# Performance work log

Hardware: AMD Instinct MI355X
Metric: run time of the kernel (lower is better)

Reference implementation:

```python
import jax, jax.numpy as jnp
import numpy as np

B, L, D = 2, 2048, 1024
E = 15        # routed experts
H = D * 1     # hidden_expansion = 1
K = 3         # active experts per token
T = 1.0       # router temperature


def setup_inputs() -> dict:
    key = jax.random.key(0)
    ks = jax.random.split(key, 12)
    s = 0.02
    return {
        "x": jax.random.normal(ks[0], (B, L, D), dtype=jnp.float32),
        "router_W": jax.random.normal(ks[1], (D, E), dtype=jnp.float32) * s,
        "router_b": jnp.zeros((E,), dtype=jnp.float32),
        "sW1": jax.random.normal(ks[2], (D, H), dtype=jnp.float32) * s,
        "sb1": jnp.zeros((H,), dtype=jnp.float32),
        "sW2": jax.random.normal(ks[3], (H, D), dtype=jnp.float32) * s,
        "sb2": jnp.zeros((D,), dtype=jnp.float32),
        "eW1": jax.random.normal(ks[4], (E, D, H), dtype=jnp.float32) * s,
        "eb1": jnp.zeros((E, H), dtype=jnp.float32),
        "eW2": jax.random.normal(ks[5], (E, H, D), dtype=jnp.float32) * s,
        "eb2": jnp.zeros((E, D), dtype=jnp.float32),
    }


def reference(x, router_W, router_b, sW1, sb1, sW2, sb2, eW1, eb1, eW2, eb2):
    b, l, d = x.shape
    n = b * l
    xt = x.reshape(n, d)                                   # [N, D] tokens

    # shared expert FFN (single shared expert)
    shared = jax.nn.relu(xt @ sW1 + sb1) @ sW2 + sb2       # [N, D]

    # router: softmax over experts with temperature, top-k selection
    logits = xt @ router_W + router_b                      # [N, E]
    probs = jax.nn.softmax(logits / T, axis=-1)
    top_p, top_i = jax.lax.top_k(probs, K)                 # [N, K]

    # combine weights: zero outside top-k
    cw = jnp.zeros((n, E), dtype=probs.dtype)
    cw = cw.at[jnp.arange(n)[:, None], top_i].set(top_p)   # [N, E]

    # routed experts (dense dispatch form of gather-FFN-scatter)
    h = jax.nn.relu(jnp.einsum('nd,edh->neh', xt, eW1) + eb1)   # [N, E, H]
    ye = jnp.einsum('neh,ehd->ned', h, eW2) + eb2               # [N, E, D]
    routed = jnp.einsum('ned,ne->nd', ye, cw)                   # [N, D]

    return (shared + routed).reshape(b, l, d)
```

## Files before the change

### kernel.cpp

```cpp
#include <hip/hip_runtime.h>
#include <hip/hip_bf16.h>

#define NTOK 4096
#define DDIM 1024
#define NEXP 15
#define KTOP 3
#define NSLOT_R (NTOK*KTOP)
#define LIST_STRIDE 4096
#define BK 32
#define NT (DDIM/BK)

typedef __attribute__((ext_vector_type(4))) float f32x4;
typedef __attribute__((ext_vector_type(8))) __bf16 bf16x8;
typedef __attribute__((ext_vector_type(4))) __bf16 bf16x4;

__device__ __forceinline__ void gload_lds16(const void* g, void* l) {
    __builtin_amdgcn_global_load_lds(
        (const __attribute__((address_space(1))) void*)g,
        (__attribute__((address_space(3))) void*)l, 16, 0, 0);
}

__global__ __launch_bounds__(256) void router_kernel(
    const float* __restrict__ x, const float* __restrict__ rW,
    const float* __restrict__ rb, int* __restrict__ cnt,
    int* __restrict__ list, float* __restrict__ wslot)
{
    const int lane = threadIdx.x & 63;
    const int wid  = threadIdx.x >> 6;
    const int n    = blockIdx.x * 4 + wid;

    float xv[16];
#pragma unroll
    for (int i = 0; i < 16; ++i) xv[i] = x[(size_t)n * DDIM + lane + 64 * i];

    float p[NEXP];
#pragma unroll
    for (int e = 0; e < NEXP; ++e) {
        float s = 0.f;
#pragma unroll
        for (int i = 0; i < 16; ++i)
            s += xv[i] * rW[(size_t)(lane + 64 * i) * NEXP + e];
#pragma unroll
        for (int off = 32; off > 0; off >>= 1) s += __shfl_xor(s, off);
        p[e] = s + rb[e];
    }
    float m = p[0];
#pragma unroll
    for (int e = 1; e < NEXP; ++e) m = fmaxf(m, p[e]);
    float Z = 0.f;
#pragma unroll
    for (int e = 0; e < NEXP; ++e) { p[e] = expf(p[e] - m); Z += p[e]; }
    const float inv = 1.f / Z;

    if (lane == 0) {
        int sel0 = -1, sel1 = -1;
        for (int k = 0; k < KTOP; ++k) {
            float best = -1.f; int bi = 0;
            for (int e = 0; e < NEXP; ++e) {
                if (e == sel0 || e == sel1) continue;
                if (p[e] > best) { best = p[e]; bi = e; }
            }
            wslot[n * KTOP + k] = best * inv;
            int pos = atomicAdd(&cnt[bi], 1);
            list[bi * LIST_STRIDE + pos] = n * KTOP + k;
            if (k == 0) sel0 = bi; else sel1 = bi;
        }
    }
}

__global__ __launch_bounds__(256) void transpose_convert(
    const float* __restrict__ eW, const float* __restrict__ sW,
    __bf16* __restrict__ dst)
{
    const int bi = blockIdx.x, bj = blockIdx.y, z = blockIdx.z;
    const float* src = (z < 15) ? eW + (size_t)z * 1024 * 1024 : sW;
    __bf16* d = dst + (size_t)z * 1024 * 1024;

    __shared__ __bf16 tile[64][66];
    const int t = threadIdx.x, c = t & 63;
#pragma unroll
    for (int i = 0; i < 16; ++i) {
        int r = i * 4 + (t >> 6);
        tile[c][r] = (__bf16)src[(size_t)(bi * 64 + r) * 1024 + bj * 64 + c];
    }
    __syncthreads();
#pragma unroll
    for (int i = 0; i < 4; ++i) {
        int rr = i * 16 + (t >> 4);
        int c4 = (t & 15) * 4;
        bf16x4 v;
#pragma unroll
        for (int q = 0; q < 4; ++q) v[q] = tile[rr][c4 + q];
        *(bf16x4*)&d[(size_t)(bj * 64 + rr) * 1024 + bi * 64 + c4] = v;
    }
}

__global__ __launch_bounds__(256) void convert_x(
    const float* __restrict__ x, __bf16* __restrict__ xb)
{
    int i = (blockIdx.x * 256 + threadIdx.x) * 4;
    f32x4 v = *(const f32x4*)&x[i];
    bf16x4 o;
#pragma unroll
    for (int q = 0; q < 4; ++q) o[q] = (__bf16)v[q];
    *(bf16x4*)&xb[i] = o;
}

template<int PASS, bool ATOMIC>
__global__ __launch_bounds__(256) void ffn_pass(
    const __bf16* __restrict__ Wt,
    const float* __restrict__ eb, const float* __restrict__ sb,
    const __bf16* __restrict__ Xsrc,
    const int* __restrict__ cnt, const int* __restrict__ list,
    const float* __restrict__ wslot,
    __bf16* __restrict__ Yout,
    float* __restrict__ out)
{
    const int st = blockIdx.x;
    const int ct = blockIdx.y;
    const int e  = blockIdx.z;
    const bool shared_e = (e == NEXP);
    const int count = shared_e ? NTOK : cnt[e];
    const int s0 = st * 128;
    if (s0 >= count) return;

    const __bf16* Wp = Wt + (size_t)e * 1024 * 1024;
    const float*  bp = shared_e ? sb : eb + (size_t)e * DDIM;

    __shared__ __bf16 Wl[3][128 * BK];
    __shared__ __bf16 Xl[3][128 * BK];

    const int tid = threadIdx.x, lane = tid & 63, w = tid >> 6;
    const int wm = w >> 1, wn = w & 1, r15 = lane & 15, g = lane >> 4;

    int srcrow[2];
#pragma unroll
    for (int i = 0; i < 2; ++i) {
        int r = min(s0 + (tid >> 2) + 64 * i, count - 1);
        if (shared_e) srcrow[i] = (PASS == 1) ? r : (NSLOT_R + r);
        else { int slot = list[e * LIST_STRIDE + r]; srcrow[i] = (PASS == 1) ? (slot / KTOP) : slot; }
    }
    const int wc   = ct * 128 + (tid >> 2);
    const int gsub = (tid & 3) * 8;

    auto stage = [&](int buf, int k0) {
#pragma unroll
        for (int i = 0; i < 2; ++i) {
            gload_lds16(&Wp[(size_t)(wc + 64 * i) * 1024 + k0 + gsub],
                        &Wl[buf][(i * 64 + w * 16) * BK]);
            gload_lds16(&Xsrc[(size_t)srcrow[i] * 1024 + k0 + gsub],
                        &Xl[buf][(i * 64 + w * 16) * BK]);
        }
    };

    f32x4 acc[4][4];
#pragma unroll
    for (int a = 0; a < 4; ++a)
#pragma unroll
        for (int b = 0; b < 4; ++b) acc[a][b] = (f32x4){0.f, 0.f, 0.f, 0.f};

    stage(0, 0);
    stage(1, BK);

    for (int t = 0; t < NT; ++t) {
        if (t + 1 < NT) asm volatile("s_waitcnt vmcnt(4)" ::: "memory");
        else            asm volatile("s_waitcnt vmcnt(0)" ::: "memory");
        __builtin_amdgcn_s_barrier();
        __builtin_amdgcn_sched_barrier(0);

        const int b0 = t % 3;
        const __bf16* Wb = &Wl[b0][0];
        const __bf16* Xb = &Xl[b0][0];
        bf16x8 wf[4], xf[4];
#pragma unroll
        for (int f = 0; f < 4; ++f) {
            wf[f] = *(const bf16x8*)&Wb[(wm * 64 + f * 16 + r15) * BK + g * 8];
            xf[f] = *(const bf16x8*)&Xb[(wn * 64 + f * 16 + r15) * BK + g * 8];
        }
        if (t + 2 < NT) stage((t + 2) % 3, (t + 2) * BK);
#pragma unroll
        for (int fm = 0; fm < 4; ++fm)
#pragma unroll
            for (int fn = 0; fn < 4; ++fn)
                acc[fm][fn] = __builtin_amdgcn_mfma_f32_16x16x32_bf16(
                    wf[fm], xf[fn], acc[fm][fn], 0, 0, 0);
    }

    int  slotg[4]; bool val[4];
#pragma unroll
    for (int fn = 0; fn < 4; ++fn) {
        int sl = s0 + wn * 64 + fn * 16 + r15;
        val[fn] = (sl < count);
        int sc = min(sl, count - 1);
        slotg[fn] = shared_e ? (NSLOT_R + sc) : list[e * LIST_STRIDE + sc];
    }

    if constexpr (!ATOMIC) {
#pragma unroll
        for (int fm = 0; fm < 4; ++fm) {
            int c0 = ct * 128 + wm * 64 + fm * 16 + g * 4;
            f32x4 bias = *(const f32x4*)&bp[c0];
#pragma unroll
            for (int fn = 0; fn < 4; ++fn) if (val[fn]) {
                bf16x4 v;
#pragma unroll
                for (int q = 0; q < 4; ++q) {
                    float y = acc[fm][fn][q] + bias[q];
                    if (PASS == 1) y = fmaxf(y, 0.f);
                    v[q] = (__bf16)y;
                }
                *(bf16x4*)&Yout[(size_t)slotg[fn] * DDIM + c0] = v;
            }
        }
    } else {
        int ntok[4]; float wgt[4];
#pragma unroll
        for (int fn = 0; fn < 4; ++fn) {
            int slot = slotg[fn];
            ntok[fn] = (slot < NSLOT_R) ? (slot / KTOP) : (slot - NSLOT_R);
            wgt[fn]  = (slot < NSLOT_R) ? wslot[slot] : 1.f;
        }
#pragma unroll
        for (int fm = 0; fm < 4; ++fm) {
            int c0 = ct * 128 + wm * 64 + fm * 16 + g * 4;
            f32x4 bias = *(const f32x4*)&bp[c0];
#pragma unroll
            for (int fn = 0; fn < 4; ++fn) if (val[fn]) {
#pragma unroll
                for (int q = 0; q < 4; ++q)
                    atomicAdd(&out[(size_t)ntok[fn] * DDIM + c0 + q],
                              wgt[fn] * (acc[fm][fn][q] + bias[q]));
            }
        }
    }
}

__global__ __launch_bounds__(256) void combine_kernel(
    const __bf16* __restrict__ ybuf, const float* __restrict__ wslot,
    float* __restrict__ out)
{
    const int idx = blockIdx.x * 256 + threadIdx.x;
    const int n   = idx >> 7;
    const int d0  = (idx & 127) * 8;
    const float w0 = wslot[n * 3 + 0];
    const float w1 = wslot[n * 3 + 1];
    const float w2 = wslot[n * 3 + 2];
    bf16x8 y0 = *(const bf16x8*)&ybuf[(size_t)(n * 3 + 0) * DDIM + d0];
    bf16x8 y1 = *(const bf16x8*)&ybuf[(size_t)(n * 3 + 1) * DDIM + d0];
    bf16x8 y2 = *(const bf16x8*)&ybuf[(size_t)(n * 3 + 2) * DDIM + d0];
    bf16x8 ys = *(const bf16x8*)&ybuf[(size_t)(NSLOT_R + n) * DDIM + d0];
    float r[8];
#pragma unroll
    for (int j = 0; j < 8; ++j)
        r[j] = w0 * (float)y0[j] + w1 * (float)y1[j] + w2 * (float)y2[j] + (float)ys[j];
    f32x4 lo = {r[0], r[1], r[2], r[3]}, hi = {r[4], r[5], r[6], r[7]};
    *(f32x4*)&out[(size_t)n * DDIM + d0]     = lo;
    *(f32x4*)&out[(size_t)n * DDIM + d0 + 4] = hi;
}

extern "C" void kernel_launch(void* const* d_in, const int* in_sizes, int n_in,
                              void* d_out, int out_size, void* d_ws, size_t ws_size,
                              hipStream_t stream) {
    const float* x   = (const float*)d_in[0];
    const float* rW  = (const float*)d_in[1];
    const float* rb  = (const float*)d_in[2];
    const float* sW1 = (const float*)d_in[3];
    const float* sb1 = (const float*)d_in[4];
    const float* sW2 = (const float*)d_in[5];
    const float* sb2 = (const float*)d_in[6];
    const float* eW1 = (const float*)d_in[7];
    const float* eb1 = (const float*)d_in[8];
    const float* eW2 = (const float*)d_in[9];
    const float* eb2 = (const float*)d_in[10];
    float* out = (float*)d_out;

    const size_t MB = 1 << 20;
    char* wsb = (char*)d_ws;
    int*    cnt   = (int*)wsb;
    int*    list  = (int*)(wsb + 256);
    float*  wslot = (float*)(wsb + (512 << 10));
    __bf16* xb    = (__bf16*)(wsb + 1 * MB);

    const dim3 ggrid(NTOK / 128, DDIM / 128, NEXP + 1);

    if (ws_size >= 105 * MB) {
        __bf16* W1t  = (__bf16*)(wsb + 9 * MB);
        __bf16* W2t  = (__bf16*)(wsb + 41 * MB);
        __bf16* hbuf = (__bf16*)(wsb + 73 * MB);
        __bf16* ybuf = (__bf16*)(wsb + 9 * MB);

        hipMemsetAsync(cnt, 0, 64, stream);
        router_kernel<<<NTOK / 4, 256, 0, stream>>>(x, rW, rb, cnt, list, wslot);
        convert_x<<<NTOK * DDIM / 1024, 256, 0, stream>>>(x, xb);
        transpose_convert<<<dim3(16, 16, 16), 256, 0, stream>>>(eW1, sW1, W1t);
        transpose_convert<<<dim3(16, 16, 16), 256, 0, stream>>>(eW2, sW2, W2t);

        ffn_pass<1, false><<<ggrid, 256, 0, stream>>>(
            W1t, eb1, sb1, xb, cnt, list, nullptr, hbuf, nullptr);
        ffn_pass<2, false><<<ggrid, 256, 0, stream>>>(
            W2t, eb2, sb2, hbuf, cnt, list, nullptr, ybuf, nullptr);
        combine_kernel<<<NTOK * 128 / 256, 256, 0, stream>>>(ybuf, wslot, out);
    } else if (ws_size >= 73 * MB) {
        __bf16* Wt   = (__bf16*)(wsb + 9 * MB);
        __bf16* hbuf = (__bf16*)(wsb + 41 * MB);

        hipMemsetAsync(cnt, 0, 64, stream);
        hipMemsetAsync(d_out, 0, (size_t)out_size * sizeof(float), stream);
        router_kernel<<<NTOK / 4, 256, 0, stream>>>(x, rW, rb, cnt, list, wslot);
        convert_x<<<NTOK * DDIM / 1024, 256, 0, stream>>>(x, xb);

        transpose_convert<<<dim3(16, 16, 16), 256, 0, stream>>>(eW1, sW1, Wt);
        ffn_pass<1, false><<<ggrid, 256, 0, stream>>>(
            Wt, eb1, sb1, xb, cnt, list, nullptr, hbuf, nullptr);
        transpose_convert<<<dim3(16, 16, 16), 256, 0, stream>>>(eW2, sW2, Wt);
        ffn_pass<2, true><<<ggrid, 256, 0, stream>>>(
            Wt, eb2, sb2, hbuf, cnt, list, wslot, nullptr, out);
    }
}
```

Before: 710.9 us.

## Enlarge FFN GEMM tile to 256 tokens, fuse x conversion into router

The grouped FFN GEMM tile grows from 128x128 to 256 token rows by 128 output columns. Each wave now computes 128x64 with 32 accumulators, and the MFMA block is raised to high priority with s_setprio. Weight tiles are reused across more tokens, cutting weight traffic and the number of blocks. The bf16 conversion of x moves into the router kernel, which already loads x, removing one launch and one read of x. The costs are more registers and LDS per block, lower occupancy, and more padding waste for experts whose token counts do not fill a 256-row tile.

```diff
diff --git a/kernel.cpp b/kernel.cpp
--- a/kernel.cpp
+++ b/kernel.cpp
@@ -9,6 +9,8 @@
 #define LIST_STRIDE 4096
 #define BK 32
 #define NT (DDIM/BK)
+#define BM 256
+#define BN 128
 
 typedef __attribute__((ext_vector_type(4))) float f32x4;
 typedef __attribute__((ext_vector_type(8))) __bf16 bf16x8;
@@ -23,7 +25,8 @@
 __global__ __launch_bounds__(256) void router_kernel(
     const float* __restrict__ x, const float* __restrict__ rW,
     const float* __restrict__ rb, int* __restrict__ cnt,
-    int* __restrict__ list, float* __restrict__ wslot)
+    int* __restrict__ list, float* __restrict__ wslot,
+    __bf16* __restrict__ xb)
 {
     const int lane = threadIdx.x & 63;
     const int wid  = threadIdx.x >> 6;
@@ -32,6 +35,10 @@
     float xv[16];
 #pragma unroll
     for (int i = 0; i < 16; ++i) xv[i] = x[(size_t)n * DDIM + lane + 64 * i];
+
+#pragma unroll
+    for (int i = 0; i < 16; ++i)
+        xb[(size_t)n * DDIM + lane + 64 * i] = (__bf16)xv[i];
 
     float p[NEXP];
 #pragma unroll
@@ -93,17 +100,6 @@
         for (int q = 0; q < 4; ++q) v[q] = tile[rr][c4 + q];
         *(bf16x4*)&d[(size_t)(bj * 64 + rr) * 1024 + bi * 64 + c4] = v;
     }
-}
-
-__global__ __launch_bounds__(256) void convert_x(
-    const float* __restrict__ x, __bf16* __restrict__ xb)
-{
-    int i = (blockIdx.x * 256 + threadIdx.x) * 4;
-    f32x4 v = *(const f32x4*)&x[i];
-    bf16x4 o;
-#pragma unroll
-    for (int q = 0; q < 4; ++q) o[q] = (__bf16)v[q];
-    *(bf16x4*)&xb[i] = o;
 }
 
 template<int PASS, bool ATOMIC>
@@ -121,41 +117,42 @@
     const int e  = blockIdx.z;
     const bool shared_e = (e == NEXP);
     const int count = shared_e ? NTOK : cnt[e];
-    const int s0 = st * 128;
+    const int s0 = st * BM;
     if (s0 >= count) return;
 
     const __bf16* Wp = Wt + (size_t)e * 1024 * 1024;
     const float*  bp = shared_e ? sb : eb + (size_t)e * DDIM;
 
-    __shared__ __bf16 Wl[3][128 * BK];
-    __shared__ __bf16 Xl[3][128 * BK];
+    __shared__ __bf16 Wl[3][BN * BK];
+    __shared__ __bf16 Xl[3][BM * BK];
 
     const int tid = threadIdx.x, lane = tid & 63, w = tid >> 6;
     const int wm = w >> 1, wn = w & 1, r15 = lane & 15, g = lane >> 4;
 
-    int srcrow[2];
-#pragma unroll
-    for (int i = 0; i < 2; ++i) {
+    int srcrow[4];
+#pragma unroll
+    for (int i = 0; i < 4; ++i) {
         int r = min(s0 + (tid >> 2) + 64 * i, count - 1);
         if (shared_e) srcrow[i] = (PASS == 1) ? r : (NSLOT_R + r);
         else { int slot = list[e * LIST_STRIDE + r]; srcrow[i] = (PASS == 1) ? (slot / KTOP) : slot; }
     }
-    const int wc   = ct * 128 + (tid >> 2);
+    const int wc   = ct * BN + (tid >> 2);
     const int gsub = (tid & 3) * 8;
 
     auto stage = [&](int buf, int k0) {
 #pragma unroll
-        for (int i = 0; i < 2; ++i) {
+        for (int i = 0; i < 2; ++i)
             gload_lds16(&Wp[(size_t)(wc + 64 * i) * 1024 + k0 + gsub],
                         &Wl[buf][(i * 64 + w * 16) * BK]);
+#pragma unroll
+        for (int i = 0; i < 4; ++i)
             gload_lds16(&Xsrc[(size_t)srcrow[i] * 1024 + k0 + gsub],
                         &Xl[buf][(i * 64 + w * 16) * BK]);
-        }
     };
 
-    f32x4 acc[4][4];
-#pragma unroll
-    for (int a = 0; a < 4; ++a)
+    f32x4 acc[8][4];
+#pragma unroll
+    for (int a = 0; a < 8; ++a)
 #pragma unroll
         for (int b = 0; b < 4; ++b) acc[a][b] = (f32x4){0.f, 0.f, 0.f, 0.f};
 
@@ -163,7 +160,7 @@
     stage(1, BK);
 
     for (int t = 0; t < NT; ++t) {
-        if (t + 1 < NT) asm volatile("s_waitcnt vmcnt(4)" ::: "memory");
+        if (t + 1 < NT) asm volatile("s_waitcnt vmcnt(6)" ::: "memory");
         else            asm volatile("s_waitcnt vmcnt(0)" ::: "memory");
         __builtin_amdgcn_s_barrier();
         __builtin_amdgcn_sched_barrier(0);
@@ -171,65 +168,68 @@
         const int b0 = t % 3;
         const __bf16* Wb = &Wl[b0][0];
         const __bf16* Xb = &Xl[b0][0];
-        bf16x8 wf[4], xf[4];
-#pragma unroll
-        for (int f = 0; f < 4; ++f) {
-            wf[f] = *(const bf16x8*)&Wb[(wm * 64 + f * 16 + r15) * BK + g * 8];
-            xf[f] = *(const bf16x8*)&Xb[(wn * 64 + f * 16 + r15) * BK + g * 8];
-        }
+        bf16x8 wf[4], xf[8];
+#pragma unroll
+        for (int f = 0; f < 4; ++f)
+            wf[f] = *(const bf16x8*)&Wb[(wn * 64 + f * 16 + r15) * BK + g * 8];
+#pragma unroll
+        for (int f = 0; f < 8; ++f)
+            xf[f] = *(const bf16x8*)&Xb[(wm * 128 + f * 16 + r15) * BK + g * 8];
         if (t + 2 < NT) stage((t + 2) % 3, (t + 2) * BK);
-#pragma unroll
-        for (int fm = 0; fm < 4; ++fm)
-#pragma unroll
-            for (int fn = 0; fn < 4; ++fn)
-                acc[fm][fn] = __builtin_amdgcn_mfma_f32_16x16x32_bf16(
-                    wf[fm], xf[fn], acc[fm][fn], 0, 0, 0);
-    }
-
-    int  slotg[4]; bool val[4];
-#pragma unroll
-    for (int fn = 0; fn < 4; ++fn) {
-        int sl = s0 + wn * 64 + fn * 16 + r15;
-        val[fn] = (sl < count);
+        __builtin_amdgcn_s_setprio(1);
+#pragma unroll
+        for (int s = 0; s < 8; ++s)
+#pragma unroll
+            for (int c = 0; c < 4; ++c)
+                acc[s][c] = __builtin_amdgcn_mfma_f32_16x16x32_bf16(
+                    wf[c], xf[s], acc[s][c], 0, 0, 0);
+        __builtin_amdgcn_s_setprio(0);
+    }
+
+    int  slotg[8]; bool val[8];
+#pragma unroll
+    for (int s = 0; s < 8; ++s) {
+        int sl = s0 + wm * 128 + s * 16 + r15;
+        val[s] = (sl < count);
         int sc = min(sl, count - 1);
-        slotg[fn] = shared_e ? (NSLOT_R + sc) : list[e * LIST_STRIDE + sc];
+        slotg[s] = shared_e ? (NSLOT_R + sc) : list[e * LIST_STRIDE + sc];
     }
 
     if constexpr (!ATOMIC) {
 #pragma unroll
-        for (int fm = 0; fm < 4; ++fm) {
-            int c0 = ct * 128 + wm * 64 + fm * 16 + g * 4;
+        for (int c = 0; c < 4; ++c) {
+            int c0 = ct * BN + wn * 64 + c * 16 + g * 4;
             f32x4 bias = *(const f32x4*)&bp[c0];
 #pragma unroll
-            for (int fn = 0; fn < 4; ++fn) if (val[fn]) {
+            for (int s = 0; s < 8; ++s) if (val[s]) {
                 bf16x4 v;
 #pragma unroll
                 for (int q = 0; q < 4; ++q) {
-                    float y = acc[fm][fn][q] + bias[q];
+                    float y = acc[s][c][q] + bias[q];
                     if (PASS == 1) y = fmaxf(y, 0.f);
                     v[q] = (__bf16)y;
                 }
-                *(bf16x4*)&Yout[(size_t)slotg[fn] * DDIM + c0] = v;
+                *(bf16x4*)&Yout[(size_t)slotg[s] * DDIM + c0] = v;
             }
         }
     } else {
-        int ntok[4]; float wgt[4];
-#pragma unroll
-        for (int fn = 0; fn < 4; ++fn) {
-            int slot = slotg[fn];
-            ntok[fn] = (slot < NSLOT_R) ? (slot / KTOP) : (slot - NSLOT_R);
-            wgt[fn]  = (slot < NSLOT_R) ? wslot[slot] : 1.f;
+        int ntok[8]; float wgt[8];
+#pragma unroll
+        for (int s = 0; s < 8; ++s) {
+            int slot = slotg[s];
+            ntok[s] = (slot < NSLOT_R) ? (slot / KTOP) : (slot - NSLOT_R);
+            wgt[s]  = (slot < NSLOT_R) ? wslot[slot] : 1.f;
         }
 #pragma unroll
-        for (int fm = 0; fm < 4; ++fm) {
-            int c0 = ct * 128 + wm * 64 + fm * 16 + g * 4;
+        for (int c = 0; c < 4; ++c) {
+            int c0 = ct * BN + wn * 64 + c * 16 + g * 4;
             f32x4 bias = *(const f32x4*)&bp[c0];
 #pragma unroll
-            for (int fn = 0; fn < 4; ++fn) if (val[fn]) {
+            for (int s = 0; s < 8; ++s) if (val[s]) {
 #pragma unroll
                 for (int q = 0; q < 4; ++q)
-                    atomicAdd(&out[(size_t)ntok[fn] * DDIM + c0 + q],
-                              wgt[fn] * (acc[fm][fn][q] + bias[q]));
+                    atomicAdd(&out[(size_t)ntok[s] * DDIM + c0 + q],
+                              wgt[s] * (acc[s][c][q] + bias[q]));
             }
         }
     }
@@ -281,7 +281,7 @@
     float*  wslot = (float*)(wsb + (512 << 10));
     __bf16* xb    = (__bf16*)(wsb + 1 * MB);
 
-    const dim3 ggrid(NTOK / 128, DDIM / 128, NEXP + 1);
+    const dim3 ggrid(NTOK / BM, DDIM / BN, NEXP + 1);
 
     if (ws_size >= 105 * MB) {
         __bf16* W1t  = (__bf16*)(wsb + 9 * MB);
@@ -290,8 +290,7 @@
         __bf16* ybuf = (__bf16*)(wsb + 9 * MB);
 
         hipMemsetAsync(cnt, 0, 64, stream);
-        router_kernel<<<NTOK / 4, 256, 0, stream>>>(x, rW, rb, cnt, list, wslot);
-        convert_x<<<NTOK * DDIM / 1024, 256, 0, stream>>>(x, xb);
+        router_kernel<<<NTOK / 4, 256, 0, stream>>>(x, rW, rb, cnt, list, wslot, xb);
         transpose_convert<<<dim3(16, 16, 16), 256, 0, stream>>>(eW1, sW1, W1t);
         transpose_convert<<<dim3(16, 16, 16), 256, 0, stream>>>(eW2, sW2, W2t);
 
@@ -306,8 +305,7 @@
 
         hipMemsetAsync(cnt, 0, 64, stream);
         hipMemsetAsync(d_out, 0, (size_t)out_size * sizeof(float), stream);
-        router_kernel<<<NTOK / 4, 256, 0, stream>>>(x, rW, rb, cnt, list, wslot);
-        convert_x<<<NTOK * DDIM / 1024, 256, 0, stream>>>(x, xb);
+        router_kernel<<<NTOK / 4, 256, 0, stream>>>(x, rW, rb, cnt, list, wslot, xb);
 
         transpose_convert<<<dim3(16, 16, 16), 256, 0, stream>>>(eW1, sW1, Wt);
         ffn_pass<1, false><<<ggrid, 256, 0, stream>>>(
```

After: 752.9 us. +5.9%, slower.
